# Performance work log

Measured on AMD Instinct MI355X. Metric: run time of the kernel, lower is better.

## Reference

```python
import jax, jax.numpy as jnp
import numpy as np

B, L, H = 512, 50, 256
N_NODE, N_CATE, N_REL, DEG = 200000, 1000, 4, 12
N = B * L          # graph nodes (seed items of the neighbor-sampled subgraph)
E = N * DEG        # sampled edges (12 neighbors per seed node)


def _layer_norm(x):
    # CARES.layer_norm: center then divide by L2 norm of the centered vector
    x = x - jnp.mean(x, -1, keepdims=True)
    return x / jnp.sqrt(jnp.sum(x * x, -1, keepdims=True))


def _ave_pool(h, gm):
    # h: [B,L,H], gm: [B,L] float
    return jnp.sum(h * gm[..., None], 1) / jnp.sum(gm, 1)[:, None]


def _session_encoder(Ws, bs, w5, Wt, bt, seq_hidden, mean_item, mean_cate, mask):
    # Ws: [4,H,H], bs: [4,H], w5: [H], Wt: [2H,H], bt: [H]
    b, l, h = seq_hidden.shape
    last = (jnp.sum(mask, 1) - 1)[:, None, None]
    ht = jnp.take_along_axis(seq_hidden, jnp.broadcast_to(last, (b, 1, h)), axis=1)[:, 0]
    q1 = (ht @ Ws[0] + bs[0])[:, None, :]
    q2 = (mean_item @ Ws[1] + bs[1])[:, None, :]
    q3 = seq_hidden @ Ws[2] + bs[2]
    q4 = (mean_cate @ Ws[3] + bs[3])[:, None, :]
    alpha = jnp.einsum('blh,h->bl', jax.nn.sigmoid(q1 + q2 + q3 + q4), w5)[..., None]
    a = jnp.sum(alpha * seq_hidden * mask[..., None].astype(seq_hidden.dtype), 1)
    return jnp.concatenate([a, ht], 1) @ Wt + bt


def _gat(x, edge_index, rel_e, edge_attr, gat_W, n_nodes):
    # relation-aware single-head GAT layer: gather -> edge attention -> segment softmax -> scatter
    h = x @ gat_W                               # [N,H]
    src, dst = edge_index[0], edge_index[1]
    msg = h[src] + rel_e                        # [E,H] relation-augmented message
    logit = jax.nn.leaky_relu(jnp.sum(h[dst] * msg, -1) / np.sqrt(h.shape[-1]).astype(np.float32), 0.2) + edge_attr
    mx = jax.ops.segment_max(logit, dst, num_segments=n_nodes)
    ex = jnp.exp(logit - mx[dst])
    den = jax.ops.segment_sum(ex, dst, num_segments=n_nodes)
    att = ex / (den[dst] + 1e-12)
    return jax.ops.segment_sum(att[:, None] * msg, dst, num_segments=n_nodes)


def setup_inputs() -> dict:
    key = jax.random.key(0)
    ks = jax.random.split(key, 20)
    s = 1.0 / np.sqrt(H)  # reset_parameters: uniform(-stdv, stdv)
    uni = lambda k, shape: jax.random.uniform(k, shape, jnp.float32, -s, s)
    return {
        'alias_inputs': jax.random.randint(ks[0], (B, L), 0, L),
        'items': jax.random.randint(ks[1], (B, L), 1, N_NODE),
        'mask': jnp.ones((B, L), jnp.int32),
        'cates': jax.random.randint(ks[2], (B, L), 0, N_CATE),
        'edge_index': jax.random.randint(ks[3], (2, E), 0, N),
        'edge_type': jax.random.randint(ks[4], (E,), 0, N_REL),
        'edge_attr': jax.random.normal(ks[5], (E,), jnp.float32) * 0.1,
        'item_emb': uni(ks[6], (N_NODE, H)),
        'cate_emb': uni(ks[7], (N_CATE, H)),
        'pos_emb': uni(ks[8], (L, H)),
        'len_emb': uni(ks[9], (2 * L, H)),
        'rel_emb': uni(ks[10], (N_REL, H)),
        'se_W': uni(ks[11], (2, 4, H, H)),   # linears one..four for the 2 SessionEncoders
        'se_b': uni(ks[12], (2, 4, H)),
        'se_w5': uni(ks[13], (2, H)),        # linear_five (H->1, no bias)
        'se_Wt': uni(ks[14], (2, 2 * H, H)), # linear_transform
        'se_bt': uni(ks[15], (2, H)),
        'gat_W': uni(ks[16], (H, H)),
    }


def reference(alias_inputs, items, mask, cates, edge_index, edge_type, edge_attr,
              item_emb, cate_emb, pos_emb, len_emb, rel_emb,
              se_W, se_b, se_w5, se_Wt, se_bt, gat_W):
    gm = jnp.sign(items).astype(jnp.float32)            # graph_mask
    hidden = item_emb[items]                            # [B,L,H]
    cate_hidden = cate_emb[cates]
    mean_item = _ave_pool(hidden, gm)
    mean_cate = _ave_pool(cate_hidden, gm)

    # h0 = hidden[i][alias_inputs[i]]
    idx = jnp.broadcast_to(alias_inputs[..., None], (B, L, H))
    h0 = jnp.take_along_axis(hidden, idx, axis=1)

    # add_pos_encoding
    pos = jnp.arange(L - 1, -1, -1)[None, :]
    len_d = jnp.sum(mask, 1, keepdims=True)             # [B,1]
    pos_index = (pos - (L - len_d)) * mask              # [B,L]
    seq_hidden = h0 + pos_emb[pos_index] + len_emb[jnp.broadcast_to(len_d, (B, L))]

    local_sess = _session_encoder(se_W[0], se_b[0], se_w5[0], se_Wt[0], se_bt[0],
                                  seq_hidden, mean_item, mean_cate, mask)

    # relation-aware GAT over the sampled subgraph
    x = item_emb[items.reshape(-1)]                     # [N,H]
    out = _gat(x, edge_index, rel_emb[edge_type], edge_attr, gat_W, N)
    graph_emb = out.reshape(B, L, H)
    s_node = _ave_pool(graph_emb, gm)

    g_seq = jnp.take_along_axis(graph_emb, idx, axis=1)
    global_sess = _session_encoder(se_W[1], se_b[1], se_w5[1], se_Wt[1], se_bt[1],
                                   g_seq, mean_item, s_node, mask)

    return _layer_norm(local_sess + global_sess)        # [B,H]
```

## Files before the change

kernel.cpp:

```cpp
#include <hip/hip_runtime.h>
#include <hip/hip_bf16.h>

#define B 512
#define L 50
#define H 256
#define GN (B*L)
#define GE (GN*12)

typedef unsigned short u16;
typedef unsigned int u32;

__device__ __forceinline__ float bf2f(u16 u){ u32 x=((u32)u)<<16; return __uint_as_float(x); }

__device__ __forceinline__ float4 load4(const void* p, size_t idx, int f32){
  if (f32) return *reinterpret_cast<const float4*>(reinterpret_cast<const float*>(p)+idx);
  ushort4 u = *reinterpret_cast<const ushort4*>(reinterpret_cast<const u16*>(p)+idx);
  return make_float4(bf2f(u.x),bf2f(u.y),bf2f(u.z),bf2f(u.w));
}
__device__ __forceinline__ float load1(const void* p, size_t idx, int f32){
  return f32 ? reinterpret_cast<const float*>(p)[idx] : bf2f(reinterpret_cast<const u16*>(p)[idx]);
}
__device__ __forceinline__ float waveSum(float v){
  #pragma unroll
  for (int m=32;m>0;m>>=1) v += __shfl_xor(v, m, 64);
  return v;
}

__global__ void k_probe(const void* emb, int* flag){
  if (threadIdx.x==0 && blockIdx.x==0){
    int big=0;
    const u16* p=(const u16*)emb;
    for (int i=0;i<256;i++){ float v=bf2f(p[i]); if(!(v==v) || fabsf(v)>4.f) big++; }
    *flag = (big>8)?1:0;
  }
}

__global__ void k_gather_hidden(const int* items, const void* item_emb, float* hidden, const int* flagp){
  int f32=*flagp;
  int n=blockIdx.x, lane=threadIdx.x;
  int idx=items[n];
  float4 v=load4(item_emb,(size_t)idx*H+lane*4,f32);
  *reinterpret_cast<float4*>(hidden+(size_t)n*H+lane*4)=v;
}

__global__ void k_means(const int* items, const int* cates, const int* mask, const float* hidden,
                        const void* cate_emb, float* mi, float* mc, float* gms, int* lend, const int* flagp){
  int f32=*flagp;
  int b=blockIdx.x, h=threadIdx.x;
  float si=0.f, sc=0.f, g=0.f; int lm=0;
  for (int l=0;l<L;l++){
    int it=items[b*L+l];
    float gm=(it>0)?1.f:((it<0)?-1.f:0.f);
    si += gm*hidden[((size_t)b*L+l)*H+h];
    int c=cates[b*L+l];
    sc += gm*load1(cate_emb,(size_t)c*H+h,f32);
    g += gm;
    lm += mask[b*L+l];
  }
  mi[(size_t)b*H+h]=si/g; mc[(size_t)b*H+h]=sc/g;
  if (h==0){ gms[b]=g; lend[b]=lm; }
}

__global__ void k_seq(const int* alias_, const int* mask, const float* hidden,
                      const void* pos_emb, const void* len_emb, const int* lend, float* seqh, const int* flagp){
  int f32=*flagp;
  int r=blockIdx.x, lane=threadIdx.x;
  int b=r/L, l=r%L;
  int a=alias_[r];
  int ld=lend[b];
  int m=mask[r];
  int pidx=(ld-1-l)*m;
  if (pidx<0) pidx+=L;
  float4 hv=*reinterpret_cast<const float4*>(hidden+((size_t)b*L+a)*H+lane*4);
  float4 pv=load4(pos_emb,(size_t)pidx*H+lane*4,f32);
  float4 lv=load4(len_emb,(size_t)ld*H+lane*4,f32);
  float4 o=make_float4(hv.x+pv.x+lv.x, hv.y+pv.y+lv.y, hv.z+pv.z+lv.z, hv.w+pv.w+lv.w);
  *reinterpret_cast<float4*>(seqh+(size_t)r*H+lane*4)=o;
}

__global__ void k_ht(const float* x, const int* lend, float* ht){
  int b=blockIdx.x, h=threadIdx.x;
  int last=lend[b]-1; if(last<0) last+=L;
  ht[(size_t)b*H+h]=x[((size_t)b*L+last)*H+h];
}

__global__ __launch_bounds__(256) void k_gemm(const float* A, const void* W, size_t wOff,
                                              float* C, const void* bias, size_t bOff,
                                              int M, int Nc, int K, int accFlag, const int* flagp){
  int f32=*flagp;
  __shared__ float At[16][68];
  __shared__ float Ws[16][64];
  int bm=blockIdx.x*64, bn=blockIdx.y*64;
  int t=threadIdx.x;
  int tx=t&15, ty=t>>4;
  float c[4][4]={};
  int r=t>>2, kq=(t&3)<<2;
  int kk=t>>4, nq=(t&15)<<2;
  for (int k0=0;k0<K;k0+=16){
    float4 av=*reinterpret_cast<const float4*>(A+(size_t)(bm+r)*K+(k0+kq));
    At[kq+0][r]=av.x; At[kq+1][r]=av.y; At[kq+2][r]=av.z; At[kq+3][r]=av.w;
    float4 wv=load4(W,wOff+(size_t)(k0+kk)*Nc+(bn+nq),f32);
    Ws[kk][nq+0]=wv.x; Ws[kk][nq+1]=wv.y; Ws[kk][nq+2]=wv.z; Ws[kk][nq+3]=wv.w;
    __syncthreads();
    #pragma unroll
    for (int q=0;q<16;q++){
      float4 a4=*reinterpret_cast<const float4*>(&At[q][ty<<2]);
      float4 w4=*reinterpret_cast<const float4*>(&Ws[q][tx<<2]);
      float aa[4]={a4.x,a4.y,a4.z,a4.w};
      float ww[4]={w4.x,w4.y,w4.z,w4.w};
      #pragma unroll
      for (int i=0;i<4;i++)
        #pragma unroll
        for (int j=0;j<4;j++) c[i][j]=fmaf(aa[i],ww[j],c[i][j]);
    }
    __syncthreads();
  }
  #pragma unroll
  for (int i=0;i<4;i++){
    size_t row=(size_t)(bm+(ty<<2)+i);
    #pragma unroll
    for (int j=0;j<4;j++){
      int col=bn+(tx<<2)+j;
      float v=c[i][j];
      if (bias) v+=load1(bias,bOff+col,f32);
      if (accFlag) v+=C[row*Nc+col];
      C[row*Nc+col]=v;
    }
  }
}

__global__ void k_alpha(const float* qb, const float* q3, const void* seb, size_t bOff,
                        const void* w5, size_t wOff, float* alpha, const int* flagp){
  int f32=*flagp;
  int gid=blockIdx.x*blockDim.x+threadIdx.x;
  int wid=gid>>6, lane=gid&63;
  if (wid>=GN) return;
  int b=wid/L;
  float4 qv=*reinterpret_cast<const float4*>(qb+(size_t)b*H+lane*4);
  float4 q3v=*reinterpret_cast<const float4*>(q3+(size_t)wid*H+lane*4);
  float bs0=0.f,bs1=0.f,bs2=0.f,bs3=0.f;
  #pragma unroll
  for (int j=0;j<4;j++){
    float4 bv=load4(seb,bOff+(size_t)j*H+lane*4,f32);
    bs0+=bv.x; bs1+=bv.y; bs2+=bv.z; bs3+=bv.w;
  }
  float4 wv=load4(w5,wOff+(size_t)lane*4,f32);
  float part=0.f;
  float x0=qv.x+q3v.x+bs0; part+=wv.x/(1.f+expf(-x0));
  float x1=qv.y+q3v.y+bs1; part+=wv.y/(1.f+expf(-x1));
  float x2=qv.z+q3v.z+bs2; part+=wv.z/(1.f+expf(-x2));
  float x3=qv.w+q3v.w+bs3; part+=wv.w/(1.f+expf(-x3));
  part=waveSum(part);
  if (lane==0) alpha[wid]=part;
}

__global__ void k_pool(const float* alpha, const float* seqh, const int* mask, const float* ht, float* cat){
  int b=blockIdx.x, h=threadIdx.x;
  float a=0.f;
  for (int l=0;l<L;l++)
    a += alpha[b*L+l]*seqh[((size_t)b*L+l)*H+h]*(float)mask[b*L+l];
  cat[(size_t)b*2*H+h]=a;
  cat[(size_t)b*2*H+H+h]=ht[(size_t)b*H+h];
}

__global__ void k_count(const int* dst, int* cnt){
  int e=blockIdx.x*blockDim.x+threadIdx.x;
  if (e<GE) atomicAdd(&cnt[dst[e]],1);
}

__global__ void k_scan(const int* cnt, int* rowp){
  __shared__ int s[1024];
  int t=threadIdx.x;
  int base=t*25;
  int local[25]; int sum=0;
  #pragma unroll
  for (int i=0;i<25;i++){ local[i]=sum; sum+=cnt[base+i]; }
  s[t]=sum; __syncthreads();
  for (int off=1;off<1024;off<<=1){
    int v=(t>=off)?s[t-off]:0; __syncthreads();
    s[t]+=v; __syncthreads();
  }
  int excl=s[t]-sum;
  #pragma unroll
  for (int i=0;i<25;i++) rowp[base+i]=excl+local[i];
  if (t==1023) rowp[GN]=s[1023];
}

__global__ void k_fill(const int* dst, const int* rowp, int* cnt, int* eord){
  int e=blockIdx.x*blockDim.x+threadIdx.x;
  if (e<GE){ int d=dst[e]; int pos=rowp[d]+atomicAdd(&cnt[d],1); eord[pos]=e; }
}

__global__ void k_node(const float* hg, const int* src, const int* etype, const void* eattr,
                       const void* rel, const int* rowp, const int* eord, float* out, const int* flagp){
  int f32=*flagp;
  int gid=blockIdx.x*blockDim.x+threadIdx.x;
  int n=gid>>6, lane=gid&63;
  if (n>=GN) return;
  float4 hn=*reinterpret_cast<const float4*>(hg+(size_t)n*H+lane*4);
  int b0=rowp[n], b1=rowp[n+1];
  float mx=-INFINITY, den=0.f;
  float4 acc=make_float4(0.f,0.f,0.f,0.f);
  for (int i=b0;i<b1;i++){
    int e=eord[i]; int s=src[e]; int ty=etype[e];
    float4 hs=*reinterpret_cast<const float4*>(hg+(size_t)s*H+lane*4);
    float4 rv=load4(rel,(size_t)ty*H+lane*4,f32);
    float4 m4=make_float4(hs.x+rv.x,hs.y+rv.y,hs.z+rv.z,hs.w+rv.w);
    float p=hn.x*m4.x+hn.y*m4.y+hn.z*m4.z+hn.w*m4.w;
    p=waveSum(p)*(1.f/16.f);
    float lg=(p>0.f?p:0.2f*p)+load1(eattr,e,f32);
    if (lg>mx){
      float sc=expf(mx-lg);
      den*=sc; acc.x*=sc; acc.y*=sc; acc.z*=sc; acc.w*=sc;
      mx=lg;
    }
    float ex=expf(lg-mx);
    den+=ex;
    acc.x+=ex*m4.x; acc.y+=ex*m4.y; acc.z+=ex*m4.z; acc.w+=ex*m4.w;
  }
  float inv=1.f/(den+1e-12f);
  float4 o=make_float4(acc.x*inv,acc.y*inv,acc.z*inv,acc.w*inv);
  *reinterpret_cast<float4*>(out+(size_t)n*H+lane*4)=o;
}

__global__ void k_avepool(const float* x, const int* items, const float* gms, float* out){
  int b=blockIdx.x, h=threadIdx.x;
  float s=0.f;
  for (int l=0;l<L;l++){
    int it=items[b*L+l];
    float gm=(it>0)?1.f:((it<0)?-1.f:0.f);
    s += gm*x[((size_t)b*L+l)*H+h];
  }
  out[(size_t)b*H+h]=s/gms[b];
}

__global__ void k_gseq(const int* alias_, const float* graph, float* gseq){
  int r=blockIdx.x, lane=threadIdx.x;
  int b=r/L;
  int a=alias_[r];
  float4 v=*reinterpret_cast<const float4*>(graph+((size_t)b*L+a)*H+lane*4);
  *reinterpret_cast<float4*>(gseq+(size_t)r*H+lane*4)=v;
}

__global__ void k_final(const float* sl, const float* sg, float* out){
  __shared__ float red[8];
  int b=blockIdx.x, h=threadIdx.x;
  int wid=h>>6, lane=h&63;
  float v=sl[(size_t)b*H+h]+sg[(size_t)b*H+h];
  float s=waveSum(v);
  if (lane==0) red[wid]=s;
  __syncthreads();
  float tot=red[0]+red[1]+red[2]+red[3];
  float x=v-tot/(float)H;
  float s2=waveSum(x*x);
  __syncthreads();
  if (lane==0) red[wid]=s2;
  __syncthreads();
  float ss=red[0]+red[1]+red[2]+red[3];
  out[(size_t)b*H+h]=x/sqrtf(ss);
}

extern "C" void kernel_launch(void* const* d_in, const int* in_sizes, int n_in,
                              void* d_out, int out_size, void* d_ws, size_t ws_size,
                              hipStream_t stream){
  (void)in_sizes; (void)n_in; (void)out_size; (void)ws_size;
  const int* alias_=(const int*)d_in[0];
  const int* items =(const int*)d_in[1];
  const int* mask  =(const int*)d_in[2];
  const int* cates =(const int*)d_in[3];
  const int* eind  =(const int*)d_in[4];
  const int* etype =(const int*)d_in[5];
  const void* eattr   =d_in[6];
  const void* item_emb=d_in[7];
  const void* cate_emb=d_in[8];
  const void* pos_emb =d_in[9];
  const void* len_emb =d_in[10];
  const void* rel_emb =d_in[11];
  const void* se_W    =d_in[12];
  const void* se_b    =d_in[13];
  const void* se_w5   =d_in[14];
  const void* se_Wt   =d_in[15];
  const void* se_bt   =d_in[16];
  const void* gat_W   =d_in[17];
  const int* esrc=eind; const int* edst=eind+GE;

  char* w=(char*)d_ws;
  auto carve=[&](size_t nbytes)->char*{ char* p=w; w += (nbytes+255)&~(size_t)255; return p; };
  float* buf1 =(float*)carve((size_t)GN*H*4);
  float* buf2 =(float*)carve((size_t)GN*H*4);
  float* hgat =(float*)carve((size_t)GN*H*4);
  float* q3   =(float*)carve((size_t)GN*H*4);
  float* alphaB=(float*)carve((size_t)GN*4);
  float* qb   =(float*)carve((size_t)B*H*4);
  float* mi   =(float*)carve((size_t)B*H*4);
  float* mc   =(float*)carve((size_t)B*H*4);
  float* sn   =(float*)carve((size_t)B*H*4);
  float* gms  =(float*)carve((size_t)B*4);
  int*   lend =(int*)  carve((size_t)B*4);
  float* htb  =(float*)carve((size_t)B*H*4);
  float* htg  =(float*)carve((size_t)B*H*4);
  float* catb =(float*)carve((size_t)B*2*H*4);
  float* sl   =(float*)carve((size_t)B*H*4);
  float* sg   =(float*)carve((size_t)B*H*4);
  int*   cnt  =(int*)  carve((size_t)GN*4);
  int*   rowp =(int*)  carve((size_t)(GN+1)*4);
  int*   eord =(int*)  carve((size_t)GE*4);
  int*   flag =(int*)  carve(256);

  dim3 blk(256), gBig(GN/64,H/64), gSm(B/64,H/64);

  k_probe<<<1,64,0,stream>>>(item_emb, flag);
  k_gather_hidden<<<GN,64,0,stream>>>(items, item_emb, buf1, flag);
  k_means<<<B,256,0,stream>>>(items,cates,mask,buf1,cate_emb,mi,mc,gms,lend,flag);
  k_seq<<<GN,64,0,stream>>>(alias_,mask,buf1,pos_emb,len_emb,lend,buf2,flag);
  k_ht<<<B,256,0,stream>>>(buf2,lend,htb);

  k_gemm<<<gBig,blk,0,stream>>>(buf1, gat_W, 0, hgat, nullptr,0, GN,H,H, 0, flag);

  k_gemm<<<gBig,blk,0,stream>>>(buf2, se_W, (size_t)2*H*H, q3, nullptr,0, GN,H,H, 0, flag);
  k_gemm<<<gSm,blk,0,stream>>>(htb, se_W, 0,             qb, nullptr,0, B,H,H, 0, flag);
  k_gemm<<<gSm,blk,0,stream>>>(mi,  se_W, (size_t)1*H*H, qb, nullptr,0, B,H,H, 1, flag);
  k_gemm<<<gSm,blk,0,stream>>>(mc,  se_W, (size_t)3*H*H, qb, nullptr,0, B,H,H, 1, flag);
  k_alpha<<<GN/4,256,0,stream>>>(qb,q3,se_b,0,se_w5,0,alphaB,flag);
  k_pool<<<B,256,0,stream>>>(alphaB,buf2,mask,htb,catb);
  k_gemm<<<gSm,blk,0,stream>>>(catb, se_Wt, 0, sl, se_bt, 0, B,H,2*H, 0, flag);

  (void)hipMemsetAsync(cnt,0,(size_t)GN*4,stream);
  k_count<<<GE/256,256,0,stream>>>(edst,cnt);
  k_scan<<<1,1024,0,stream>>>(cnt,rowp);
  (void)hipMemsetAsync(cnt,0,(size_t)GN*4,stream);
  k_fill<<<GE/256,256,0,stream>>>(edst,rowp,cnt,eord);
  k_node<<<GN/4,256,0,stream>>>(hgat,esrc,etype,eattr,rel_emb,rowp,eord,buf1,flag);

  k_avepool<<<B,256,0,stream>>>(buf1,items,gms,sn);
  k_gseq<<<GN,64,0,stream>>>(alias_,buf1,buf2);
  k_ht<<<B,256,0,stream>>>(buf2,lend,htg);
  k_gemm<<<gBig,blk,0,stream>>>(buf2, se_W, (size_t)6*H*H, q3, nullptr,0, GN,H,H, 0, flag);
  k_gemm<<<gSm,blk,0,stream>>>(htg, se_W, (size_t)4*H*H, qb, nullptr,0, B,H,H, 0, flag);
  k_gemm<<<gSm,blk,0,stream>>>(mi,  se_W, (size_t)5*H*H, qb, nullptr,0, B,H,H, 1, flag);
  k_gemm<<<gSm,blk,0,stream>>>(sn,  se_W, (size_t)7*H*H, qb, nullptr,0, B,H,H, 1, flag);
  k_alpha<<<GN/4,256,0,stream>>>(qb,q3,se_b,(size_t)4*H,se_w5,(size_t)H,alphaB,flag);
  k_pool<<<B,256,0,stream>>>(alphaB,buf2,mask,htg,catb);
  k_gemm<<<gSm,blk,0,stream>>>(catb, se_Wt, (size_t)2*H*H, sg, se_bt, (size_t)H, B,H,2*H, 0, flag);

  k_final<<<B,256,0,stream>>>(sl,sg,(float*)d_out);
}
```

Baseline: 868.0 us.

## Drop dtype probe, fuse gather with means, ht into seq, and fuse query GEMMs

Removes the runtime bf16/fp32 probe kernel and all per-load dtype branching, so inputs are always read as fp32. It fuses the item-embedding gather into the means kernel and folds the last-item (ht) extraction into the seq/gseq kernels. It also merges the three small query GEMMs plus bias sums into one kernel, which drops the read-modify-write accumulation and the bias loads from the alpha kernel. Together these cut launch count and redundant traffic. The risk is that bf16 inputs are no longer supported, and k_gather_means now gathers embeddings with a less coalesced access pattern.

```diff
diff --git a/kernel.cpp b/kernel.cpp
--- a/kernel.cpp
+++ b/kernel.cpp
@@ -1,5 +1,4 @@
 #include <hip/hip_runtime.h>
-#include <hip/hip_bf16.h>
 
 #define B 512
 #define L 50
@@ -7,53 +6,25 @@
 #define GN (B*L)
 #define GE (GN*12)
 
-typedef unsigned short u16;
-typedef unsigned int u32;
-
-__device__ __forceinline__ float bf2f(u16 u){ u32 x=((u32)u)<<16; return __uint_as_float(x); }
-
-__device__ __forceinline__ float4 load4(const void* p, size_t idx, int f32){
-  if (f32) return *reinterpret_cast<const float4*>(reinterpret_cast<const float*>(p)+idx);
-  ushort4 u = *reinterpret_cast<const ushort4*>(reinterpret_cast<const u16*>(p)+idx);
-  return make_float4(bf2f(u.x),bf2f(u.y),bf2f(u.z),bf2f(u.w));
-}
-__device__ __forceinline__ float load1(const void* p, size_t idx, int f32){
-  return f32 ? reinterpret_cast<const float*>(p)[idx] : bf2f(reinterpret_cast<const u16*>(p)[idx]);
-}
 __device__ __forceinline__ float waveSum(float v){
   #pragma unroll
   for (int m=32;m>0;m>>=1) v += __shfl_xor(v, m, 64);
   return v;
 }
-
-__global__ void k_probe(const void* emb, int* flag){
-  if (threadIdx.x==0 && blockIdx.x==0){
-    int big=0;
-    const u16* p=(const u16*)emb;
-    for (int i=0;i<256;i++){ float v=bf2f(p[i]); if(!(v==v) || fabsf(v)>4.f) big++; }
-    *flag = (big>8)?1:0;
-  }
-}
-
-__global__ void k_gather_hidden(const int* items, const void* item_emb, float* hidden, const int* flagp){
-  int f32=*flagp;
-  int n=blockIdx.x, lane=threadIdx.x;
-  int idx=items[n];
-  float4 v=load4(item_emb,(size_t)idx*H+lane*4,f32);
-  *reinterpret_cast<float4*>(hidden+(size_t)n*H+lane*4)=v;
-}
-
-__global__ void k_means(const int* items, const int* cates, const int* mask, const float* hidden,
-                        const void* cate_emb, float* mi, float* mc, float* gms, int* lend, const int* flagp){
-  int f32=*flagp;
+__device__ __forceinline__ float sigm(float x){ return 1.f/(1.f+expf(-x)); }
+
+__global__ void k_gather_means(const int* items, const int* cates, const int* mask,
+                               const float* item_emb, const float* cate_emb,
+                               float* hidden, float* mi, float* mc, float* gms, int* lend){
   int b=blockIdx.x, h=threadIdx.x;
   float si=0.f, sc=0.f, g=0.f; int lm=0;
   for (int l=0;l<L;l++){
     int it=items[b*L+l];
     float gm=(it>0)?1.f:((it<0)?-1.f:0.f);
-    si += gm*hidden[((size_t)b*L+l)*H+h];
-    int c=cates[b*L+l];
-    sc += gm*load1(cate_emb,(size_t)c*H+h,f32);
+    float v=item_emb[(size_t)it*H+h];
+    hidden[((size_t)b*L+l)*H+h]=v;
+    si += gm*v;
+    sc += gm*cate_emb[(size_t)cates[b*L+l]*H+h];
     g += gm;
     lm += mask[b*L+l];
   }
@@ -62,8 +33,8 @@
 }
 
 __global__ void k_seq(const int* alias_, const int* mask, const float* hidden,
-                      const void* pos_emb, const void* len_emb, const int* lend, float* seqh, const int* flagp){
-  int f32=*flagp;
+                      const float* pos_emb, const float* len_emb, const int* lend,
+                      float* seqh, float* ht){
   int r=blockIdx.x, lane=threadIdx.x;
   int b=r/L, l=r%L;
   int a=alias_[r];
@@ -72,22 +43,17 @@
   int pidx=(ld-1-l)*m;
   if (pidx<0) pidx+=L;
   float4 hv=*reinterpret_cast<const float4*>(hidden+((size_t)b*L+a)*H+lane*4);
-  float4 pv=load4(pos_emb,(size_t)pidx*H+lane*4,f32);
-  float4 lv=load4(len_emb,(size_t)ld*H+lane*4,f32);
+  float4 pv=*reinterpret_cast<const float4*>(pos_emb+(size_t)pidx*H+lane*4);
+  float4 lv=*reinterpret_cast<const float4*>(len_emb+(size_t)ld*H+lane*4);
   float4 o=make_float4(hv.x+pv.x+lv.x, hv.y+pv.y+lv.y, hv.z+pv.z+lv.z, hv.w+pv.w+lv.w);
   *reinterpret_cast<float4*>(seqh+(size_t)r*H+lane*4)=o;
-}
-
-__global__ void k_ht(const float* x, const int* lend, float* ht){
-  int b=blockIdx.x, h=threadIdx.x;
-  int last=lend[b]-1; if(last<0) last+=L;
-  ht[(size_t)b*H+h]=x[((size_t)b*L+last)*H+h];
-}
-
-__global__ __launch_bounds__(256) void k_gemm(const float* A, const void* W, size_t wOff,
-                                              float* C, const void* bias, size_t bOff,
-                                              int M, int Nc, int K, int accFlag, const int* flagp){
-  int f32=*flagp;
+  if (l == (ld+L-1)%L)
+    *reinterpret_cast<float4*>(ht+(size_t)b*H+lane*4)=o;
+}
+
+__global__ __launch_bounds__(256) void k_gemm(const float* A, const float* W, size_t wOff,
+                                              float* C, const float* bias, size_t bOff,
+                                              int M, int Nc, int K){
   __shared__ float At[16][68];
   __shared__ float Ws[16][64];
   int bm=blockIdx.x*64, bn=blockIdx.y*64;
@@ -99,7 +65,7 @@
   for (int k0=0;k0<K;k0+=16){
     float4 av=*reinterpret_cast<const float4*>(A+(size_t)(bm+r)*K+(k0+kq));
     At[kq+0][r]=av.x; At[kq+1][r]=av.y; At[kq+2][r]=av.z; At[kq+3][r]=av.w;
-    float4 wv=load4(W,wOff+(size_t)(k0+kk)*Nc+(bn+nq),f32);
+    float4 wv=*reinterpret_cast<const float4*>(W+wOff+(size_t)(k0+kk)*Nc+(bn+nq));
     Ws[kk][nq+0]=wv.x; Ws[kk][nq+1]=wv.y; Ws[kk][nq+2]=wv.z; Ws[kk][nq+3]=wv.w;
     __syncthreads();
     #pragma unroll
@@ -122,34 +88,73 @@
     for (int j=0;j<4;j++){
       int col=bn+(tx<<2)+j;
       float v=c[i][j];
-      if (bias) v+=load1(bias,bOff+col,f32);
-      if (accFlag) v+=C[row*Nc+col];
+      if (bias) v+=bias[bOff+col];
       C[row*Nc+col]=v;
     }
   }
 }
 
-__global__ void k_alpha(const float* qb, const float* q3, const void* seb, size_t bOff,
-                        const void* w5, size_t wOff, float* alpha, const int* flagp){
-  int f32=*flagp;
+__global__ __launch_bounds__(256) void k_qb3(const float* A0, const float* A1, const float* A2,
+                                             const float* W, size_t wBase,
+                                             const float* seb, size_t bOff, float* C){
+  __shared__ float At[16][68];
+  __shared__ float Ws[16][64];
+  int bm=blockIdx.x*64, bn=blockIdx.y*64;
+  int t=threadIdx.x;
+  int tx=t&15, ty=t>>4;
+  float c[4][4]={};
+  int r=t>>2, kq=(t&3)<<2;
+  int kk=t>>4, nq=(t&15)<<2;
+  const float* As[3]={A0,A1,A2};
+  const int widx[3]={0,1,3};
+  for (int src=0;src<3;src++){
+    const float* A=As[src];
+    size_t wOff=wBase+(size_t)widx[src]*H*H;
+    for (int k0=0;k0<H;k0+=16){
+      float4 av=*reinterpret_cast<const float4*>(A+(size_t)(bm+r)*H+(k0+kq));
+      At[kq+0][r]=av.x; At[kq+1][r]=av.y; At[kq+2][r]=av.z; At[kq+3][r]=av.w;
+      float4 wv=*reinterpret_cast<const float4*>(W+wOff+(size_t)(k0+kk)*H+(bn+nq));
+      Ws[kk][nq+0]=wv.x; Ws[kk][nq+1]=wv.y; Ws[kk][nq+2]=wv.z; Ws[kk][nq+3]=wv.w;
+      __syncthreads();
+      #pragma unroll
+      for (int q=0;q<16;q++){
+        float4 a4=*reinterpret_cast<const float4*>(&At[q][ty<<2]);
+        float4 w4=*reinterpret_cast<const float4*>(&Ws[q][tx<<2]);
+        float aa[4]={a4.x,a4.y,a4.z,a4.w};
+        float ww[4]={w4.x,w4.y,w4.z,w4.w};
+        #pragma unroll
+        for (int i=0;i<4;i++)
+          #pragma unroll
+          for (int j=0;j<4;j++) c[i][j]=fmaf(aa[i],ww[j],c[i][j]);
+      }
+      __syncthreads();
+    }
+  }
+  #pragma unroll
+  for (int i=0;i<4;i++){
+    size_t row=(size_t)(bm+(ty<<2)+i);
+    #pragma unroll
+    for (int j=0;j<4;j++){
+      int col=bn+(tx<<2)+j;
+      float v=c[i][j]
+        + seb[bOff+0*H+col] + seb[bOff+1*H+col]
+        + seb[bOff+2*H+col] + seb[bOff+3*H+col];
+      C[row*H+col]=v;
+    }
+  }
+}
+
+__global__ void k_alpha(const float* qb, const float* q3, const float* w5, size_t wOff,
+                        float* alpha){
   int gid=blockIdx.x*blockDim.x+threadIdx.x;
   int wid=gid>>6, lane=gid&63;
   if (wid>=GN) return;
   int b=wid/L;
   float4 qv=*reinterpret_cast<const float4*>(qb+(size_t)b*H+lane*4);
   float4 q3v=*reinterpret_cast<const float4*>(q3+(size_t)wid*H+lane*4);
-  float bs0=0.f,bs1=0.f,bs2=0.f,bs3=0.f;
-  #pragma unroll
-  for (int j=0;j<4;j++){
-    float4 bv=load4(seb,bOff+(size_t)j*H+lane*4,f32);
-    bs0+=bv.x; bs1+=bv.y; bs2+=bv.z; bs3+=bv.w;
-  }
-  float4 wv=load4(w5,wOff+(size_t)lane*4,f32);
-  float part=0.f;
-  float x0=qv.x+q3v.x+bs0; part+=wv.x/(1.f+expf(-x0));
-  float x1=qv.y+q3v.y+bs1; part+=wv.y/(1.f+expf(-x1));
-  float x2=qv.z+q3v.z+bs2; part+=wv.z/(1.f+expf(-x2));
-  float x3=qv.w+q3v.w+bs3; part+=wv.w/(1.f+expf(-x3));
+  float4 wv=*reinterpret_cast<const float4*>(w5+wOff+(size_t)lane*4);
+  float part = wv.x*sigm(qv.x+q3v.x) + wv.y*sigm(qv.y+q3v.y)
+             + wv.z*sigm(qv.z+q3v.z) + wv.w*sigm(qv.w+q3v.w);
   part=waveSum(part);
   if (lane==0) alpha[wid]=part;
 }
@@ -191,9 +196,8 @@
   if (e<GE){ int d=dst[e]; int pos=rowp[d]+atomicAdd(&cnt[d],1); eord[pos]=e; }
 }
 
-__global__ void k_node(const float* hg, const int* src, const int* etype, const void* eattr,
-                       const void* rel, const int* rowp, const int* eord, float* out, const int* flagp){
-  int f32=*flagp;
+__global__ void k_node(const float* hg, const int* src, const int* etype, const float* eattr,
+                       const float* rel, const int* rowp, const int* eord, float* out){
   int gid=blockIdx.x*blockDim.x+threadIdx.x;
   int n=gid>>6, lane=gid&63;
   if (n>=GN) return;
@@ -204,11 +208,11 @@
   for (int i=b0;i<b1;i++){
     int e=eord[i]; int s=src[e]; int ty=etype[e];
     float4 hs=*reinterpret_cast<const float4*>(hg+(size_t)s*H+lane*4);
-    float4 rv=load4(rel,(size_t)ty*H+lane*4,f32);
+    float4 rv=*reinterpret_cast<const float4*>(rel+(size_t)ty*H+lane*4);
     float4 m4=make_float4(hs.x+rv.x,hs.y+rv.y,hs.z+rv.z,hs.w+rv.w);
     float p=hn.x*m4.x+hn.y*m4.y+hn.z*m4.z+hn.w*m4.w;
     p=waveSum(p)*(1.f/16.f);
-    float lg=(p>0.f?p:0.2f*p)+load1(eattr,e,f32);
+    float lg=(p>0.f?p:0.2f*p)+eattr[e];
     if (lg>mx){
       float sc=expf(mx-lg);
       den*=sc; acc.x*=sc; acc.y*=sc; acc.z*=sc; acc.w*=sc;
@@ -234,12 +238,15 @@
   out[(size_t)b*H+h]=s/gms[b];
 }
 
-__global__ void k_gseq(const int* alias_, const float* graph, float* gseq){
+__global__ void k_gseq(const int* alias_, const float* graph, const int* lend, float* gseq, float* ht){
   int r=blockIdx.x, lane=threadIdx.x;
-  int b=r/L;
+  int b=r/L, l=r%L;
   int a=alias_[r];
   float4 v=*reinterpret_cast<const float4*>(graph+((size_t)b*L+a)*H+lane*4);
   *reinterpret_cast<float4*>(gseq+(size_t)r*H+lane*4)=v;
+  int ld=lend[b];
+  if (l == (ld+L-1)%L)
+    *reinterpret_cast<float4*>(ht+(size_t)b*H+lane*4)=v;
 }
 
 __global__ void k_final(const float* sl, const float* sg, float* out){
@@ -270,18 +277,18 @@
   const int* cates =(const int*)d_in[3];
   const int* eind  =(const int*)d_in[4];
   const int* etype =(const int*)d_in[5];
-  const void* eattr   =d_in[6];
-  const void* item_emb=d_in[7];
-  const void* cate_emb=d_in[8];
-  const void* pos_emb =d_in[9];
-  const void* len_emb =d_in[10];
-  const void* rel_emb =d_in[11];
-  const void* se_W    =d_in[12];
-  const void* se_b    =d_in[13];
-  const void* se_w5   =d_in[14];
-  const void* se_Wt   =d_in[15];
-  const void* se_bt   =d_in[16];
-  const void* gat_W   =d_in[17];
+  const float* eattr   =(const float*)d_in[6];
+  const float* item_emb=(const float*)d_in[7];
+  const float* cate_emb=(const float*)d_in[8];
+  const float* pos_emb =(const float*)d_in[9];
+  const float* len_emb =(const float*)d_in[10];
+  const float* rel_emb =(const float*)d_in[11];
+  const float* se_W    =(const float*)d_in[12];
+  const float* se_b    =(const float*)d_in[13];
+  const float* se_w5   =(const float*)d_in[14];
+  const float* se_Wt   =(const float*)d_in[15];
+  const float* se_bt   =(const float*)d_in[16];
+  const float* gat_W   =(const float*)d_in[17];
   const int* esrc=eind; const int* edst=eind+GE;
 
   char* w=(char*)d_ws;
@@ -305,43 +312,34 @@
   int*   cnt  =(int*)  carve((size_t)GN*4);
   int*   rowp =(int*)  carve((size_t)(GN+1)*4);
   int*   eord =(int*)  carve((size_t)GE*4);
-  int*   flag =(int*)  carve(256);
 
   dim3 blk(256), gBig(GN/64,H/64), gSm(B/64,H/64);
 
-  k_probe<<<1,64,0,stream>>>(item_emb, flag);
-  k_gather_hidden<<<GN,64,0,stream>>>(items, item_emb, buf1, flag);
-  k_means<<<B,256,0,stream>>>(items,cates,mask,buf1,cate_emb,mi,mc,gms,lend,flag);
-  k_seq<<<GN,64,0,stream>>>(alias_,mask,buf1,pos_emb,len_emb,lend,buf2,flag);
-  k_ht<<<B,256,0,stream>>>(buf2,lend,htb);
-
-  k_gemm<<<gBig,blk,0,stream>>>(buf1, gat_W, 0, hgat, nullptr,0, GN,H,H, 0, flag);
-
-  k_gemm<<<gBig,blk,0,stream>>>(buf2, se_W, (size_t)2*H*H, q3, nullptr,0, GN,H,H, 0, flag);
-  k_gemm<<<gSm,blk,0,stream>>>(htb, se_W, 0,             qb, nullptr,0, B,H,H, 0, flag);
-  k_gemm<<<gSm,blk,0,stream>>>(mi,  se_W, (size_t)1*H*H, qb, nullptr,0, B,H,H, 1, flag);
-  k_gemm<<<gSm,blk,0,stream>>>(mc,  se_W, (size_t)3*H*H, qb, nullptr,0, B,H,H, 1, flag);
-  k_alpha<<<GN/4,256,0,stream>>>(qb,q3,se_b,0,se_w5,0,alphaB,flag);
+  k_gather_means<<<B,256,0,stream>>>(items,cates,mask,item_emb,cate_emb,buf1,mi,mc,gms,lend);
+  k_seq<<<GN,64,0,stream>>>(alias_,mask,buf1,pos_emb,len_emb,lend,buf2,htb);
+
+  k_gemm<<<gBig,blk,0,stream>>>(buf1, gat_W, 0, hgat, nullptr,0, GN,H,H);
+
+  k_gemm<<<gBig,blk,0,stream>>>(buf2, se_W, (size_t)2*H*H, q3, nullptr,0, GN,H,H);
+  k_qb3<<<gSm,blk,0,stream>>>(htb, mi, mc, se_W, 0, se_b, 0, qb);
+  k_alpha<<<GN/4,256,0,stream>>>(qb,q3,se_w5,0,alphaB);
   k_pool<<<B,256,0,stream>>>(alphaB,buf2,mask,htb,catb);
-  k_gemm<<<gSm,blk,0,stream>>>(catb, se_Wt, 0, sl, se_bt, 0, B,H,2*H, 0, flag);
+  k_gemm<<<gSm,blk,0,stream>>>(catb, se_Wt, 0, sl, se_bt, 0, B,H,2*H);
 
   (void)hipMemsetAsync(cnt,0,(size_t)GN*4,stream);
   k_count<<<GE/256,256,0,stream>>>(edst,cnt);
   k_scan<<<1,1024,0,stream>>>(cnt,rowp);
   (void)hipMemsetAsync(cnt,0,(size_t)GN*4,stream);
   k_fill<<<GE/256,256,0,stream>>>(edst,rowp,cnt,eord);
-  k_node<<<GN/4,256,0,stream>>>(hgat,esrc,etype,eattr,rel_emb,rowp,eord,buf1,flag);
+  k_node<<<GN/4,256,0,stream>>>(hgat,esrc,etype,eattr,rel_emb,rowp,eord,buf1);
 
   k_avepool<<<B,256,0,stream>>>(buf1,items,gms,sn);
-  k_gseq<<<GN,64,0,stream>>>(alias_,buf1,buf2);
-  k_ht<<<B,256,0,stream>>>(buf2,lend,htg);
-  k_gemm<<<gBig,blk,0,stream>>>(buf2, se_W, (size_t)6*H*H, q3, nullptr,0, GN,H,H, 0, flag);
-  k_gemm<<<gSm,blk,0,stream>>>(htg, se_W, (size_t)4*H*H, qb, nullptr,0, B,H,H, 0, flag);
-  k_gemm<<<gSm,blk,0,stream>>>(mi,  se_W, (size_t)5*H*H, qb, nullptr,0, B,H,H, 1, flag);
-  k_gemm<<<gSm,blk,0,stream>>>(sn,  se_W, (size_t)7*H*H, qb, nullptr,0, B,H,H, 1, flag);
-  k_alpha<<<GN/4,256,0,stream>>>(qb,q3,se_b,(size_t)4*H,se_w5,(size_t)H,alphaB,flag);
+  k_gseq<<<GN,64,0,stream>>>(alias_,buf1,lend,buf2,htg);
+  k_gemm<<<gBig,blk,0,stream>>>(buf2, se_W, (size_t)6*H*H, q3, nullptr,0, GN,H,H);
+  k_qb3<<<gSm,blk,0,stream>>>(htg, mi, sn, se_W, (size_t)4*H*H, se_b, (size_t)4*H, qb);
+  k_alpha<<<GN/4,256,0,stream>>>(qb,q3,se_w5,(size_t)H,alphaB);
   k_pool<<<B,256,0,stream>>>(alphaB,buf2,mask,htg,catb);
-  k_gemm<<<gSm,blk,0,stream>>>(catb, se_Wt, (size_t)2*H*H, sg, se_bt, (size_t)H, B,H,2*H, 0, flag);
+  k_gemm<<<gSm,blk,0,stream>>>(catb, se_Wt, (size_t)2*H*H, sg, se_bt, (size_t)H, B,H,2*H);
 
   k_final<<<B,256,0,stream>>>(sl,sg,(float*)d_out);
 }
```

Measured after the change: 818.0 us. -5.8%, faster.
